# Performance work log

Measured on AMD Instinct MI355X. Metric: run time of the kernel, lower is better.

Reference implementation:

```python
import jax, jax.numpy as jnp
import numpy as np

COMMITMENT_COST = 0.25


def setup_inputs() -> dict:
    key = jax.random.key(0)
    k1, k2 = jax.random.split(key)
    inputs = jax.random.normal(k1, (16, 256, 32, 32), dtype=jnp.float32)
    embedding = jax.random.normal(k2, (8192, 256), dtype=jnp.float32)
    return {"inputs": inputs, "embedding": embedding}


def reference(inputs, embedding):
    # inputs: [B, C, H, W] with C == embedding_dim; embedding: [K, C]
    B, C, H, W = inputs.shape
    x = jnp.transpose(inputs, (0, 2, 3, 1))          # [B, H, W, C]
    flat = x.reshape(-1, C)                           # [N, C]
    # squared L2 distances: ||f||^2 + ||e||^2 - 2 f.e
    dist = (jnp.sum(flat * flat, axis=1, keepdims=True)
            + jnp.sum(embedding * embedding, axis=1)
            - 2.0 * flat @ embedding.T)               # [N, K]
    idx = jnp.argmin(dist, axis=1)                    # [N]
    quantized = embedding[idx].reshape(x.shape)       # [B, H, W, C]
    # commitment loss (eval mode: no EMA buffer updates)
    e_latent_loss = jnp.mean((jax.lax.stop_gradient(quantized) - x) ** 2)
    loss = COMMITMENT_COST * e_latent_loss
    # straight-through estimator
    q_st = x + jax.lax.stop_gradient(quantized - x)
    out = jnp.transpose(q_st, (0, 3, 1, 2))           # [B, C, H, W]
    return out, loss, idx.reshape(B, -1)
```

## Files before the change

### kernel.cpp

```cpp
#include <hip/hip_runtime.h>

#define C_   256
#define HW_  1024
#define N_   16384
#define K_   8192
#define OUT_SZ   4194304
#define LOSS_OFF 4194304
#define IDX_OFF  4194305
#define MARGIN   0.3f

typedef __attribute__((ext_vector_type(8)))  short short8;
typedef __attribute__((ext_vector_type(4)))  float f32x4;

#define REC_OFF    0u
#define CNORM_OFF  8388608u
#define NCNORM_OFF 8421376u
#define WS_NEED    8454144u

#define FB_CNORM   0u
#define FB_BESTS   32768u
#define FB_BESTK   557056u
#define FB_FIDX    1081344u

__device__ __forceinline__ unsigned short f2bf_rne(float x) {
  unsigned u = __float_as_uint(x);
  unsigned r = (u + 0x7fffu + ((u >> 16) & 1u)) >> 16;
  return (unsigned short)r;
}
__device__ __forceinline__ float bf2f(unsigned short h) {
  return __uint_as_float(((unsigned)h) << 16);
}
__device__ __forceinline__ void gld16(const void* g, void* l) {
  __builtin_amdgcn_global_load_lds((const __attribute__((address_space(1))) unsigned*)g,
                                   (__attribute__((address_space(3))) unsigned*)l, 16, 0, 0);
}
__device__ __forceinline__ float med3(float a, float b, float c) {
#if __has_builtin(__builtin_amdgcn_fmed3f)
  return __builtin_amdgcn_fmed3f(a, b, c);
#else
  return fmaxf(fminf(fmaxf(a, b), c), fminf(a, b));
#endif
}

__global__ __launch_bounds__(256) void conv_fused(const float* __restrict__ inp,
                                                  const float* __restrict__ emb,
                                                  unsigned short* __restrict__ Ah,
                                                  unsigned short* __restrict__ Bh,
                                                  float* __restrict__ cnorm,
                                                  float* __restrict__ ncnorm,
                                                  float* __restrict__ loss_slot) {
  __shared__ float T[64][65];
  int tid = threadIdx.x;
  if (blockIdx.x < 2048) {
    int wave = tid >> 6, lane = tid & 63;
    int k = blockIdx.x * 4 + wave;
    float4 v = *(const float4*)(emb + (size_t)k * C_ + lane * 4);
    float ss = v.x*v.x + v.y*v.y + v.z*v.z + v.w*v.w;
    #pragma unroll
    for (int m = 32; m > 0; m >>= 1) ss += __shfl_xor(ss, m);
    if (lane == 0) { cnorm[k] = 0.5f * ss; ncnorm[k] = -0.5f * ss; }
    uint2 p;
    p.x = (unsigned)f2bf_rne(v.x) | ((unsigned)f2bf_rne(v.y) << 16);
    p.y = (unsigned)f2bf_rne(v.z) | ((unsigned)f2bf_rne(v.w) << 16);
    *(uint2*)&Bh[(size_t)k * C_ + lane * 4] = p;
    if (blockIdx.x == 0 && tid == 0) { *loss_slot = 0.0f; }
  } else {
    int bb = blockIdx.x - 2048;
    int nt = bb >> 2, ct = bb & 3;
    int n0 = nt * 64, c0 = ct * 64;
    int b = n0 >> 10, hw0 = n0 & 1023;
    const float* base = inp + (size_t)b * (C_ * HW_) + hw0;
    #pragma unroll
    for (int i = 0; i < 4; ++i) {
      int cl = i * 16 + (tid >> 4);
      int h4 = (tid & 15) * 4;
      float4 v = *(const float4*)(base + (size_t)(c0 + cl) * HW_ + h4);
      T[h4 + 0][cl] = v.x; T[h4 + 1][cl] = v.y;
      T[h4 + 2][cl] = v.z; T[h4 + 3][cl] = v.w;
    }
    __syncthreads();
    #pragma unroll
    for (int jp = 0; jp < 2; ++jp) {
      int g = jp * 256 + tid;
      int nl = g >> 3, ch = (g & 7) * 8;
      unsigned short s8[8];
      #pragma unroll
      for (int k = 0; k < 8; ++k) s8[k] = f2bf_rne(T[nl][ch + k]);
      *(uint4*)&Ah[(size_t)(n0 + nl) * C_ + c0 + ch] = *(uint4*)s8;
    }
  }
}

__global__ __launch_bounds__(256, 2) void k_gemm1p(const unsigned short* __restrict__ Ah,
                                                   const unsigned short* __restrict__ Bh,
                                                   const float* __restrict__ ncnorm,
                                                   uint4* __restrict__ Rec) {
  __shared__ __align__(16) unsigned short LDS[3][12288];
  __shared__ __align__(16) float ncnL[1024];
  __shared__ float mS[2][128][3];

  const int tid = threadIdx.x, lane = tid & 63, wave = tid >> 6;
  const int wr = wave >> 1, wc = wave & 1;
  const int bid = (int)blockIdx.x;
  const int wg = (bid & 7) * 128 + (bid >> 3);
  const int rb = wg >> 3, kb = wg & 7;
  const int row0 = rb * 128;
  const int qm = lane & 15, quad = lane >> 4;
  const int sw = (quad ^ ((qm >> 1) & 3)) * 8;

  const char* srcA[2]; int dstA[2];
  #pragma unroll
  for (int t = 0; t < 2; ++t) {
    int g = t * 256 + tid;
    int row = g >> 2, chs = g & 3, ch = chs ^ ((row >> 1) & 3);
    srcA[t] = (const char*)Ah + (size_t)(row0 + row) * 512 + ch * 16;
    dstA[t] = g * 16;
  }
  const char* srcB[4]; int dstB[4];
  #pragma unroll
  for (int t = 0; t < 4; ++t) {
    int g = t * 256 + tid;
    int r = g >> 2, chs = g & 3, ch = chs ^ ((r >> 1) & 3);
    srcB[t] = (const char*)Bh + (size_t)(kb * 1024 + r) * 512 + ch * 16;
    dstB[t] = 8192 + g * 16;
  }

  gld16((const char*)ncnorm + (size_t)kb * 4096 + tid * 16, (char*)ncnL + tid * 16);
  #pragma unroll
  for (int t = 0; t < 2; ++t) gld16(srcA[t], (char*)LDS[0] + dstA[t]);
  #pragma unroll
  for (int t = 0; t < 4; ++t) gld16(srcB[t], (char*)LDS[0] + dstB[t]);
  #pragma unroll
  for (int t = 0; t < 2; ++t) gld16(srcA[t] + 64, (char*)LDS[1] + dstA[t]);
  #pragma unroll
  for (int t = 0; t < 4; ++t) gld16(srcB[t] + 64, (char*)LDS[1] + dstB[t]);
  asm volatile("s_waitcnt vmcnt(12)" ::: "memory");
  __builtin_amdgcn_s_barrier();

  const unsigned wq  = (unsigned)(wc * 128 + quad * 4);
  const unsigned kmk = 0xFFFFFF00u;

  int cur = 0, nst = 2;

  for (int sub = 0; sub < 4; ++sub) {
    const int nbe = kb * 4 + sub;
    const int nb4 = sub * 256 + wc * 128 + quad * 4;
    f32x4 acc[4][8];
    {
      float4 ncn[8];
      #pragma unroll
      for (int ct = 0; ct < 8; ++ct) ncn[ct] = *(const float4*)&ncnL[nb4 + ct * 16];
      #pragma unroll
      for (int r = 0; r < 4; ++r)
        #pragma unroll
        for (int c = 0; c < 8; ++c) {
          acc[r][c][0] = ncn[c].x; acc[r][c][1] = ncn[c].y;
          acc[r][c][2] = ncn[c].z; acc[r][c][3] = ncn[c].w;
        }
    }

    #pragma unroll 2
    for (int ci = 0; ci < 8; ++ci) {
      const int it = (sub << 3) | ci;
      if (it < 31) asm volatile("s_waitcnt vmcnt(6)" ::: "memory");
      else         asm volatile("s_waitcnt vmcnt(0)" ::: "memory");
      __builtin_amdgcn_s_barrier();
      __builtin_amdgcn_sched_barrier(0);

      if (it + 2 < 32) {
        const int nt2 = it + 2, nsub = nt2 >> 3, nci = nt2 & 7;
        #pragma unroll
        for (int t = 0; t < 2; ++t)
          gld16(srcA[t] + nci * 64, (char*)LDS[nst] + dstA[t]);
        #pragma unroll
        for (int t = 0; t < 4; ++t)
          gld16(srcB[t] + (size_t)nsub * 131072 + nci * 64, (char*)LDS[nst] + dstB[t]);
      }

      const unsigned short* Lb = &LDS[cur][0];
      short8 ah[4];
      #pragma unroll
      for (int rt = 0; rt < 4; ++rt) {
        int row = (wr * 4 + rt) * 16 + qm;
        ah[rt] = *(const short8*)&Lb[row * 32 + sw];
      }
      __builtin_amdgcn_s_setprio(1);
      #pragma unroll
      for (int ch2 = 0; ch2 < 2; ++ch2) {
        short8 bh[4];
        #pragma unroll
        for (int q = 0; q < 4; ++q) {
          int ct = ch2 * 4 + q;
          int r = (wc * 8 + ct) * 16 + qm;
          bh[q] = *(const short8*)&Lb[4096 + r * 32 + sw];
        }
        #pragma unroll
        for (int rt = 0; rt < 4; ++rt)
          #pragma unroll
          for (int q = 0; q < 4; ++q)
            acc[rt][ch2 * 4 + q] =
              __builtin_amdgcn_mfma_f32_16x16x32_bf16(bh[q], ah[rt], acc[rt][ch2 * 4 + q], 0, 0, 0);
      }
      __builtin_amdgcn_s_setprio(0);
      cur = (cur == 2) ? 0 : cur + 1;
      nst = (nst == 2) ? 0 : nst + 1;
    }

    #pragma unroll
    for (int rt = 0; rt < 4; ++rt) {
      float t1 = -3.4e38f, t2 = t1, t3 = t1;
      #pragma unroll
      for (int ct = 0; ct < 8; ++ct)
        #pragma unroll
        for (int rg = 0; rg < 4; ++rg) {
          unsigned idxv = wq | (unsigned)(ct * 16 + rg);
          float kf = __uint_as_float((__float_as_uint(acc[rt][ct][rg]) & kmk) | idxv);
          float n3 = med3(t2, kf, t3);
          float n2 = med3(t1, kf, t2);
          t1 = fmaxf(t1, kf);
          t2 = n2; t3 = n3;
        }
      #pragma unroll
      for (int m = 16; m < 64; m <<= 1) {
        float b1 = __shfl_xor(t1, m), b2 = __shfl_xor(t2, m), b3 = __shfl_xor(t3, m);
        float n3 = med3(t2, b1, t3);
        float n2 = med3(t1, b1, t2);
        t1 = fmaxf(t1, b1); t2 = n2; t3 = n3;
        n3 = med3(t2, b2, t3); t2 = fmaxf(t2, b2); t3 = n3;
        t3 = fmaxf(t3, b3);
      }
      if (quad == 0) {
        int rowl = wr * 64 + rt * 16 + qm;
        mS[wc][rowl][0] = t1; mS[wc][rowl][1] = t2; mS[wc][rowl][2] = t3;
      }
    }
    asm volatile("s_waitcnt lgkmcnt(0)" ::: "memory");
    __builtin_amdgcn_s_barrier();
    __builtin_amdgcn_sched_barrier(0);
    if (tid < 128) {
      float s1 = mS[0][tid][0], s2 = mS[0][tid][1], s3 = mS[0][tid][2];
      float b1 = mS[1][tid][0], b2 = mS[1][tid][1], b3 = mS[1][tid][2];
      float n3 = med3(s2, b1, s3);
      float n2 = med3(s1, b1, s2);
      s1 = fmaxf(s1, b1); s2 = n2; s3 = n3;
      n3 = med3(s2, b2, s3); s2 = fmaxf(s2, b2); s3 = n3;
      s3 = fmaxf(s3, b3);
      unsigned u1 = __float_as_uint(s1), u2 = __float_as_uint(s2), u3 = __float_as_uint(s3);
      uint4 rec;
      rec.x = u1 & kmk;
      rec.y = ((unsigned)f2bf_rne(__uint_as_float(u2 & kmk)) << 16)
            |  (unsigned)f2bf_rne(__uint_as_float(u3 & kmk));
      rec.z = (u1 & 255u) | ((u2 & 255u) << 8) | ((u3 & 255u) << 16);
      rec.w = 0u;
      Rec[(size_t)nbe * N_ + row0 + tid] = rec;
    }
  }
}

__global__ __launch_bounds__(256) void k_post(const float* __restrict__ inp,
                                              const float* __restrict__ emb,
                                              const float* __restrict__ cnorm,
                                              const uint4* __restrict__ Rec,
                                              float* __restrict__ out,
                                              float* __restrict__ outIdx,
                                              float* __restrict__ loss) {
  __shared__ float Q[16][258];
  __shared__ float gS[16];
  __shared__ int   ridx[16];
  __shared__ int   flist[16];
  __shared__ int   ckw[4][96];
  __shared__ float cscw[4][96];
  __shared__ int   ncw[4];
  __shared__ int   nflag;
  __shared__ float red[4];

  const int tid = threadIdx.x;
  const int n0 = blockIdx.x * 16, b = n0 >> 10, hw0 = n0 & 1023;
  const int lane = tid & 63, wv = tid >> 6;

  const int r = tid >> 4, j = tid & 15;
  const int row = n0 + r;
  uint4 rv[2];
  rv[0] = Rec[(size_t)(2 * j)     * N_ + row];
  rv[1] = Rec[(size_t)(2 * j + 1) * N_ + row];
  float m1 = -3.4e38f; int gk = 0x7fffffff;
  #pragma unroll
  for (int q = 0; q < 2; ++q) {
    float s1 = __uint_as_float(rv[q].x);
    int  kk = (2 * j + q) * 256 + (int)(rv[q].z & 255u);
    if (s1 > m1) { m1 = s1; gk = kk; }
  }
  #pragma unroll
  for (int m = 1; m < 16; m <<= 1) {
    float so = __shfl_xor(m1, m); int ko = __shfl_xor(gk, m);
    if (so > m1 || (so == m1 && ko < gk)) { m1 = so; gk = ko; }
  }
  float thr = m1 - MARGIN;
  int cnt = 0;
  #pragma unroll
  for (int q = 0; q < 2; ++q) {
    uint4 v = rv[q];
    cnt += (__uint_as_float(v.x) >= thr);
    cnt += (bf2f((unsigned short)(v.y >> 16)) >= thr);
    cnt += (bf2f((unsigned short)(v.y & 0xffffu)) >= thr);
  }
  #pragma unroll
  for (int m = 1; m < 16; m <<= 1) cnt += __shfl_xor(cnt, m);
  if (tid == 0) nflag = 0;
  __syncthreads();
  if (j == 0) {
    gS[r] = m1;
    if (cnt == 1) { ridx[r] = gk; }
    else { int p = atomicAdd(&nflag, 1); flist[p] = r; }
  }
  __syncthreads();

  int nf = nflag;
  for (int i = wv; i < nf; i += 4) {
    int lr = flist[i];
    int rw = n0 + lr;
    float fr[4];
    #pragma unroll
    for (int k = 0; k < 4; ++k)
      fr[k] = inp[(size_t)b * (C_ * HW_) + (size_t)(lane * 4 + k) * HW_ + (rw & 1023)];
    float th2 = gS[lr] - MARGIN;
    if (lane == 0) ncw[wv] = 0;
    if (lane < 32) {
      uint4 v = Rec[(size_t)lane * N_ + rw];
      float s1 = __uint_as_float(v.x);
      float s2 = bf2f((unsigned short)(v.y >> 16));
      float s3 = bf2f((unsigned short)(v.y & 0xffffu));
      int bb = lane * 256;
      if (s1 >= th2) { int p = atomicAdd(&ncw[wv], 1); ckw[wv][p] = bb + (int)(v.z & 255u); }
      if (s2 >= th2) { int p = atomicAdd(&ncw[wv], 1); ckw[wv][p] = bb + (int)((v.z >> 8) & 255u); }
      if (s3 >= th2) { int p = atomicAdd(&ncw[wv], 1); ckw[wv][p] = bb + (int)((v.z >> 16) & 255u); }
    }
    int nc = ncw[wv];
    for (int c = 0; c < nc; ++c) {
      int k = ckw[wv][c];
      float4 e = ((const float4*)(emb + (size_t)k * C_))[lane];
      float d = fr[0]*e.x + fr[1]*e.y + fr[2]*e.z + fr[3]*e.w;
      #pragma unroll
      for (int m = 32; m > 0; m >>= 1) d += __shfl_xor(d, m);
      if (lane == 0) cscw[wv][c] = d - cnorm[k];
    }
    if (lane == 0) {
      float bs = cscw[wv][0]; int bk = ckw[wv][0];
      for (int c = 1; c < nc; ++c)
        if (cscw[wv][c] > bs || (cscw[wv][c] == bs && ckw[wv][c] < bk)) { bs = cscw[wv][c]; bk = ckw[wv][c]; }
      ridx[lr] = bk;
    }
  }
  __syncthreads();

  if (tid < 16) outIdx[n0 + tid] = (float)ridx[tid];
  #pragma unroll
  for (int p = 0; p < 4; ++p) {
    int g = p * 256 + tid;
    int rr = g >> 6, c4 = (g & 63) * 4;
    int kq = ridx[rr];
    *(float4*)&Q[rr][c4] = *(const float4*)(emb + (size_t)kq * C_ + c4);
  }
  __syncthreads();

  float lsum = 0.0f;
  const int hw4 = (tid & 3) * 4, cl = tid >> 2;
  #pragma unroll
  for (int p = 0; p < 4; ++p) {
    int c = p * 64 + cl;
    size_t a = (size_t)b * (C_ * HW_) + (size_t)c * HW_ + hw0 + hw4;
    float4 x = *(const float4*)(inp + a);
    float4 q;
    q.x = Q[hw4 + 0][c]; q.y = Q[hw4 + 1][c];
    q.z = Q[hw4 + 2][c]; q.w = Q[hw4 + 3][c];
    *(float4*)(out + a) = q;
    float d0 = q.x - x.x, d1 = q.y - x.y, d2 = q.z - x.z, d3 = q.w - x.w;
    lsum += d0*d0 + d1*d1 + d2*d2 + d3*d3;
  }
  #pragma unroll
  for (int m = 32; m > 0; m >>= 1) lsum += __shfl_xor(lsum, m);
  if ((tid & 63) == 0) red[tid >> 6] = lsum;
  __syncthreads();
  if (tid == 0)
    atomicAdd(loss, (red[0] + red[1] + red[2] + red[3]) * (0.25f / (float)OUT_SZ));
}

__global__ __launch_bounds__(256) void k_norms_fb(const float* __restrict__ emb,
                                                  float* __restrict__ cnorm,
                                                  float* __restrict__ loss_slot) {
  int tid = threadIdx.x, wave = tid >> 6, lane = tid & 63;
  int k = blockIdx.x * 4 + wave;
  float4 v = *(const float4*)(emb + k * C_ + lane * 4);
  float s = v.x*v.x + v.y*v.y + v.z*v.z + v.w*v.w;
  #pragma unroll
  for (int m = 32; m > 0; m >>= 1) s += __shfl_xor(s, m);
  if (lane == 0) cnorm[k] = 0.5f * s;
  if (blockIdx.x == 0 && tid == 0) *loss_slot = 0.0f;
}

__global__ __launch_bounds__(256) void k_score_fb(const float* __restrict__ inp,
                                                  const float* __restrict__ emb,
                                                  const float* __restrict__ cnorm,
                                                  float* __restrict__ bestS,
                                                  int*   __restrict__ bestK) {
  __shared__ float As[16][132];
  __shared__ float Bs[16][132];
  const int tid = threadIdx.x;
  const int tx = tid & 15, ty = tid >> 4;
  const int rt = blockIdx.x >> 3, ks = blockIdx.x & 7;
  const int row0 = rt * 128;
  const float* Abase = inp + (row0 >> 10) * (C_ * HW_) + (row0 & 1023);
  const int kbase = ks * 1024;
  const int m4  = (tid & 31) << 2;
  const int ccA = tid >> 5;
  const int cc4 = (tid & 3) << 2;
  const int kkB = tid >> 2;

  float rS[8]; int rK[8];
  #pragma unroll
  for (int r = 0; r < 8; ++r) { rS[r] = -3.4e38f; rK[r] = 0; }

  for (int kt = 0; kt < 8; ++kt) {
    const int k0 = kbase + kt * 128;
    float acc[8][8];
    #pragma unroll
    for (int r = 0; r < 8; ++r)
      #pragma unroll
      for (int c = 0; c < 8; ++c) acc[r][c] = 0.f;

    for (int ci = 0; ci < 16; ++ci) {
      const int c0 = ci * 16;
      __syncthreads();
      #pragma unroll
      for (int p = 0; p < 2; ++p) {
        int cc = ccA + p * 8;
        float4 v = *(const float4*)(Abase + (c0 + cc) * HW_ + m4);
        *(float4*)(&As[cc][m4]) = v;
      }
      #pragma unroll
      for (int p = 0; p < 2; ++p) {
        int k = kkB + p * 64;
        float4 v = *(const float4*)(emb + (size_t)(k0 + k) * C_ + c0 + cc4);
        Bs[cc4 + 0][k] = v.x; Bs[cc4 + 1][k] = v.y;
        Bs[cc4 + 2][k] = v.z; Bs[cc4 + 3][k] = v.w;
      }
      __syncthreads();
      #pragma unroll
      for (int cc = 0; cc < 16; ++cc) {
        float4 a0 = *(const float4*)(&As[cc][ty * 8]);
        float4 a1 = *(const float4*)(&As[cc][ty * 8 + 4]);
        float4 b0 = *(const float4*)(&Bs[cc][tx * 8]);
        float4 b1 = *(const float4*)(&Bs[cc][tx * 8 + 4]);
        float a[8] = {a0.x, a0.y, a0.z, a0.w, a1.x, a1.y, a1.z, a1.w};
        float b[8] = {b0.x, b0.y, b0.z, b0.w, b1.x, b1.y, b1.z, b1.w};
        #pragma unroll
        for (int r = 0; r < 8; ++r)
          #pragma unroll
          for (int c = 0; c < 8; ++c) acc[r][c] += a[r] * b[c];
      }
    }
    float cn[8];
    {
      float4 c0v = *(const float4*)(cnorm + k0 + tx * 8);
      float4 c1v = *(const float4*)(cnorm + k0 + tx * 8 + 4);
      cn[0] = c0v.x; cn[1] = c0v.y; cn[2] = c0v.z; cn[3] = c0v.w;
      cn[4] = c1v.x; cn[5] = c1v.y; cn[6] = c1v.z; cn[7] = c1v.w;
    }
    #pragma unroll
    for (int r = 0; r < 8; ++r)
      #pragma unroll
      for (int c = 0; c < 8; ++c) {
        float s = acc[r][c] - cn[c];
        if (s > rS[r]) { rS[r] = s; rK[r] = k0 + tx * 8 + c; }
      }
  }
  #pragma unroll
  for (int r = 0; r < 8; ++r) {
    float s = rS[r]; int kk = rK[r];
    #pragma unroll
    for (int m = 1; m < 16; m <<= 1) {
      float so = __shfl_xor(s, m);
      int   ko = __shfl_xor(kk, m);
      if (so > s || (so == s && ko < kk)) { s = so; kk = ko; }
    }
    if (tx == 0) {
      int row = row0 + ty * 8 + r;
      bestS[ks * N_ + row] = s;
      bestK[ks * N_ + row] = kk;
    }
  }
}

__global__ __launch_bounds__(256) void k_merge_fb(const float* __restrict__ bestS,
                                                  const int*   __restrict__ bestK,
                                                  float* __restrict__ out_idx,
                                                  int*   __restrict__ fidx) {
  int n = blockIdx.x * 256 + threadIdx.x;
  float bs = -3.4e38f; int bk = 0x7fffffff;
  #pragma unroll
  for (int s = 0; s < 8; ++s) {
    float v = bestS[s * N_ + n];
    int  kk = bestK[s * N_ + n];
    if (v > bs || (v == bs && kk < bk)) { bs = v; bk = kk; }
  }
  out_idx[n] = (float)bk;
  fidx[n] = bk;
}

__global__ __launch_bounds__(256) void k_out_fb(const float* __restrict__ inp,
                                                const float* __restrict__ emb,
                                                const int* __restrict__ fidx,
                                                float* __restrict__ out,
                                                float* __restrict__ loss) {
  __shared__ float Q[32][260];
  int tid = threadIdx.x;
  int n0 = blockIdx.x * 32, b = n0 >> 10, hw0 = n0 & 1023;
  #pragma unroll
  for (int p = 0; p < 8; ++p) {
    int r = p * 4 + (tid >> 6);
    int kq = fidx[n0 + r];
    float4 v = *(const float4*)(emb + (size_t)kq * C_ + (tid & 63) * 4);
    *(float4*)&Q[r][(tid & 63) * 4] = v;
  }
  __syncthreads();
  int hwl = tid & 31, cl = tid >> 5;
  float lsum = 0.0f;
  #pragma unroll
  for (int p = 0; p < 32; ++p) {
    int c = p * 8 + cl;
    size_t a = (size_t)b * (C_ * HW_) + (size_t)c * HW_ + hw0 + hwl;
    float q = Q[hwl][c];
    float x = inp[a];
    out[a] = q;
    float dd = q - x; lsum += dd * dd;
  }
  #pragma unroll
  for (int m = 32; m > 0; m >>= 1) lsum += __shfl_xor(lsum, m);
  __shared__ float red[4];
  if ((tid & 63) == 0) red[tid >> 6] = lsum;
  __syncthreads();
  if (tid == 0)
    atomicAdd(loss, (red[0] + red[1] + red[2] + red[3]) * (0.25f / (float)OUT_SZ));
}

extern "C" void kernel_launch(void* const* d_in, const int* in_sizes, int n_in,
                              void* d_out, int out_size, void* d_ws, size_t ws_size,
                              hipStream_t stream) {
  const float* inp = (const float*)d_in[0];
  const float* emb = (const float*)d_in[1];
  float* out = (float*)d_out;
  char* ws = (char*)d_ws;

  if (ws_size >= (size_t)WS_NEED) {
    unsigned short* Ah = (unsigned short*)d_out;
    unsigned short* Bh = (unsigned short*)((char*)d_out + 8388608u);
    uint4* Rec     = (uint4*)(ws + REC_OFF);
    float* cnorm   = (float*)(ws + CNORM_OFF);
    float* ncnorm  = (float*)(ws + NCNORM_OFF);

    conv_fused <<<3072,  256, 0, stream>>>(inp, emb, Ah, Bh, cnorm, ncnorm,
                                           out + LOSS_OFF);
    k_gemm1p   <<<1024,  256, 0, stream>>>(Ah, Bh, ncnorm, Rec);
    k_post     <<<N_/16, 256, 0, stream>>>(inp, emb, cnorm, Rec, out,
                                           out + IDX_OFF, out + LOSS_OFF);
  } else {
    float* cnorm = (float*)(ws + FB_CNORM);
    float* bestS = (float*)(ws + FB_BESTS);
    int*   bestK = (int*)(ws + FB_BESTK);
    int*   fidx  = (int*)(ws + FB_FIDX);

    k_norms_fb <<<K_ / 4, 256, 0, stream>>>(emb, cnorm, out + LOSS_OFF);
    k_score_fb <<<1024,   256, 0, stream>>>(inp, emb, cnorm, bestS, bestK);
    k_merge_fb <<<N_/256, 256, 0, stream>>>(bestS, bestK, out + IDX_OFF, fidx);
    k_out_fb   <<<OUT_SZ/8192, 256, 0, stream>>>(inp, emb, fidx, out, out + LOSS_OFF);
  }
}
```

Baseline: 181.4 us.

## Compute commitment loss algebraically from input norms and best scores

The loss is now computed as sum ||x||^2 (accumulated in the transpose/convert kernel) minus twice the winning score, using ||q-x||^2 = ||x||^2 - 2(x.q - ||q||^2/2). This removes the re-read of the input in k_post. The k_post row-argmax reduction is also remapped so that rows lie across lanes and groups across waves, with an LDS merge step. The loss slot is now zeroed with a memset before the first kernel. In exchange, the loss for unambiguous rows uses the bf16/approximate GEMM score instead of an exact recompute, which risks precision error, and the change adds an extra memset launch.

```diff
diff --git a/kernel.cpp b/kernel.cpp
--- a/kernel.cpp
+++ b/kernel.cpp
@@ -48,8 +48,9 @@
                                                   unsigned short* __restrict__ Bh,
                                                   float* __restrict__ cnorm,
                                                   float* __restrict__ ncnorm,
-                                                  float* __restrict__ loss_slot) {
+                                                  float* __restrict__ loss) {
   __shared__ float T[64][65];
+  __shared__ float red[4];
   int tid = threadIdx.x;
   if (blockIdx.x < 2048) {
     int wave = tid >> 6, lane = tid & 63;
@@ -63,22 +64,28 @@
     p.x = (unsigned)f2bf_rne(v.x) | ((unsigned)f2bf_rne(v.y) << 16);
     p.y = (unsigned)f2bf_rne(v.z) | ((unsigned)f2bf_rne(v.w) << 16);
     *(uint2*)&Bh[(size_t)k * C_ + lane * 4] = p;
-    if (blockIdx.x == 0 && tid == 0) { *loss_slot = 0.0f; }
   } else {
     int bb = blockIdx.x - 2048;
     int nt = bb >> 2, ct = bb & 3;
     int n0 = nt * 64, c0 = ct * 64;
     int b = n0 >> 10, hw0 = n0 & 1023;
     const float* base = inp + (size_t)b * (C_ * HW_) + hw0;
+    float xsq = 0.0f;
     #pragma unroll
     for (int i = 0; i < 4; ++i) {
       int cl = i * 16 + (tid >> 4);
       int h4 = (tid & 15) * 4;
       float4 v = *(const float4*)(base + (size_t)(c0 + cl) * HW_ + h4);
+      xsq += v.x*v.x + v.y*v.y + v.z*v.z + v.w*v.w;
       T[h4 + 0][cl] = v.x; T[h4 + 1][cl] = v.y;
       T[h4 + 2][cl] = v.z; T[h4 + 3][cl] = v.w;
     }
+    #pragma unroll
+    for (int m = 32; m > 0; m >>= 1) xsq += __shfl_xor(xsq, m);
+    if ((tid & 63) == 0) red[tid >> 6] = xsq;
     __syncthreads();
+    if (tid == 0)
+      atomicAdd(loss, (red[0] + red[1] + red[2] + red[3]) * (0.25f / (float)OUT_SZ));
     #pragma unroll
     for (int jp = 0; jp < 2; ++jp) {
       int g = jp * 256 + tid;
@@ -265,53 +272,67 @@
                                               float* __restrict__ outIdx,
                                               float* __restrict__ loss) {
   __shared__ float Q[16][258];
+  __shared__ float wS[4][16];
+  __shared__ int   wK[4][16];
   __shared__ float gS[16];
+  __shared__ int   gK[16];
+  __shared__ int   sCnt[16];
+  __shared__ float sFin[16];
   __shared__ int   ridx[16];
   __shared__ int   flist[16];
   __shared__ int   ckw[4][96];
   __shared__ float cscw[4][96];
   __shared__ int   ncw[4];
   __shared__ int   nflag;
-  __shared__ float red[4];
 
   const int tid = threadIdx.x;
-  const int n0 = blockIdx.x * 16, b = n0 >> 10, hw0 = n0 & 1023;
+  const int n0 = blockIdx.x * 16, b = n0 >> 10;
   const int lane = tid & 63, wv = tid >> 6;
 
-  const int r = tid >> 4, j = tid & 15;
-  const int row = n0 + r;
-  uint4 rv[2];
-  rv[0] = Rec[(size_t)(2 * j)     * N_ + row];
-  rv[1] = Rec[(size_t)(2 * j + 1) * N_ + row];
-  float m1 = -3.4e38f; int gk = 0x7fffffff;
-  #pragma unroll
-  for (int q = 0; q < 2; ++q) {
-    float s1 = __uint_as_float(rv[q].x);
-    int  kk = (2 * j + q) * 256 + (int)(rv[q].z & 255u);
-    if (s1 > m1) { m1 = s1; gk = kk; }
-  }
-  #pragma unroll
-  for (int m = 1; m < 16; m <<= 1) {
+  const int r = tid & 15, g = tid >> 4;
+  uint4 rv0 = Rec[(size_t)(2 * g)     * N_ + n0 + r];
+  uint4 rv1 = Rec[(size_t)(2 * g + 1) * N_ + n0 + r];
+  float m1; int gk;
+  {
+    float s0 = __uint_as_float(rv0.x), s1 = __uint_as_float(rv1.x);
+    int  k0 = (2 * g) * 256 + (int)(rv0.z & 255u);
+    int  k1 = (2 * g + 1) * 256 + (int)(rv1.z & 255u);
+    m1 = s0; gk = k0;
+    if (s1 > m1) { m1 = s1; gk = k1; }
+  }
+  #pragma unroll
+  for (int m = 16; m < 64; m <<= 1) {
     float so = __shfl_xor(m1, m); int ko = __shfl_xor(gk, m);
     if (so > m1 || (so == m1 && ko < gk)) { m1 = so; gk = ko; }
   }
-  float thr = m1 - MARGIN;
-  int cnt = 0;
-  #pragma unroll
-  for (int q = 0; q < 2; ++q) {
-    uint4 v = rv[q];
-    cnt += (__uint_as_float(v.x) >= thr);
-    cnt += (bf2f((unsigned short)(v.y >> 16)) >= thr);
-    cnt += (bf2f((unsigned short)(v.y & 0xffffu)) >= thr);
-  }
-  #pragma unroll
-  for (int m = 1; m < 16; m <<= 1) cnt += __shfl_xor(cnt, m);
   if (tid == 0) nflag = 0;
-  __syncthreads();
-  if (j == 0) {
-    gS[r] = m1;
-    if (cnt == 1) { ridx[r] = gk; }
-    else { int p = atomicAdd(&nflag, 1); flist[p] = r; }
+  if (lane < 16) { wS[wv][r] = m1; wK[wv][r] = gk; }
+  __syncthreads();
+  if (tid < 16) {
+    float bm = wS[0][tid]; int bk = wK[0][tid];
+    #pragma unroll
+    for (int w = 1; w < 4; ++w) {
+      float so = wS[w][tid]; int ko = wK[w][tid];
+      if (so > bm || (so == bm && ko < bk)) { bm = so; bk = ko; }
+    }
+    gS[tid] = bm; gK[tid] = bk; sCnt[tid] = 0;
+  }
+  __syncthreads();
+  {
+    float thr = gS[r] - MARGIN;
+    int cnt = 0;
+    cnt += (__uint_as_float(rv0.x) >= thr);
+    cnt += (bf2f((unsigned short)(rv0.y >> 16)) >= thr);
+    cnt += (bf2f((unsigned short)(rv0.y & 0xffffu)) >= thr);
+    cnt += (__uint_as_float(rv1.x) >= thr);
+    cnt += (bf2f((unsigned short)(rv1.y >> 16)) >= thr);
+    cnt += (bf2f((unsigned short)(rv1.y & 0xffffu)) >= thr);
+    if (cnt) atomicAdd(&sCnt[r], cnt);
+  }
+  __syncthreads();
+  if (tid < 16) {
+    if (sCnt[tid] == 1) { ridx[tid] = gK[tid]; sFin[tid] = gS[tid]; }
+    else { int p = atomicAdd(&nflag, 1); flist[p] = tid; }
   }
   __syncthreads();
 
@@ -348,41 +369,38 @@
       float bs = cscw[wv][0]; int bk = ckw[wv][0];
       for (int c = 1; c < nc; ++c)
         if (cscw[wv][c] > bs || (cscw[wv][c] == bs && ckw[wv][c] < bk)) { bs = cscw[wv][c]; bk = ckw[wv][c]; }
-      ridx[lr] = bk;
-    }
-  }
-  __syncthreads();
-
-  if (tid < 16) outIdx[n0 + tid] = (float)ridx[tid];
+      ridx[lr] = bk; sFin[lr] = bs;
+    }
+  }
+  __syncthreads();
+
+  if (tid < 16) {
+    outIdx[n0 + tid] = (float)ridx[tid];
+    float sv = sFin[tid];
+    #pragma unroll
+    for (int m = 1; m < 16; m <<= 1) sv += __shfl_xor(sv, m);
+    if (tid == 0) atomicAdd(loss, sv * (-0.5f / (float)OUT_SZ));
+  }
   #pragma unroll
   for (int p = 0; p < 4; ++p) {
-    int g = p * 256 + tid;
-    int rr = g >> 6, c4 = (g & 63) * 4;
+    int gg = p * 256 + tid;
+    int rr = gg >> 6, c4 = (gg & 63) * 4;
     int kq = ridx[rr];
     *(float4*)&Q[rr][c4] = *(const float4*)(emb + (size_t)kq * C_ + c4);
   }
   __syncthreads();
 
-  float lsum = 0.0f;
   const int hw4 = (tid & 3) * 4, cl = tid >> 2;
+  const int hw0 = n0 & 1023;
   #pragma unroll
   for (int p = 0; p < 4; ++p) {
     int c = p * 64 + cl;
     size_t a = (size_t)b * (C_ * HW_) + (size_t)c * HW_ + hw0 + hw4;
-    float4 x = *(const float4*)(inp + a);
     float4 q;
     q.x = Q[hw4 + 0][c]; q.y = Q[hw4 + 1][c];
     q.z = Q[hw4 + 2][c]; q.w = Q[hw4 + 3][c];
     *(float4*)(out + a) = q;
-    float d0 = q.x - x.x, d1 = q.y - x.y, d2 = q.z - x.z, d3 = q.w - x.w;
-    lsum += d0*d0 + d1*d1 + d2*d2 + d3*d3;
-  }
-  #pragma unroll
-  for (int m = 32; m > 0; m >>= 1) lsum += __shfl_xor(lsum, m);
-  if ((tid & 63) == 0) red[tid >> 6] = lsum;
-  __syncthreads();
-  if (tid == 0)
-    atomicAdd(loss, (red[0] + red[1] + red[2] + red[3]) * (0.25f / (float)OUT_SZ));
+  }
 }
 
 __global__ __launch_bounds__(256) void k_norms_fb(const float* __restrict__ emb,
@@ -558,6 +576,8 @@
     float* cnorm   = (float*)(ws + CNORM_OFF);
     float* ncnorm  = (float*)(ws + NCNORM_OFF);
 
+    hipMemsetAsync((void*)(out + LOSS_OFF), 0, sizeof(float), stream);
+
     conv_fused <<<3072,  256, 0, stream>>>(inp, emb, Ah, Bh, cnorm, ncnorm,
                                            out + LOSS_OFF);
     k_gemm1p   <<<1024,  256, 0, stream>>>(Ah, Bh, ncnorm, Rec);
```

After: 190.8 us. +5.2%, slower.

## Enlarge distance GEMM tile to 256 rows with 8 waves and split-phase loads

Applied to the files above, without the earlier changes.

The distance GEMM workgroup grows from 256 to 512 threads, and its row tile grows from 128 to 256, so each loaded codebook tile is reused across twice as many input rows. The goal is to cut global and LDS traffic per MFMA. The inner loop is rewritten into two halves. Each half issues its share of the next-stage global-to-LDS copies (A, then B) between explicit barriers and LDS waits, interleaved with manually unrolled MFMA blocks. The cost is a larger LDS footprint, about 106 KB per block, which likely allows only one block per CU. It also adds two extra barriers per K step, which could expose latency.

```diff
diff --git a/kernel.cpp b/kernel.cpp
--- a/kernel.cpp
+++ b/kernel.cpp
@@ -91,50 +91,51 @@
   }
 }
 
-__global__ __launch_bounds__(256, 2) void k_gemm1p(const unsigned short* __restrict__ Ah,
+__global__ __launch_bounds__(512, 2) void k_gemm1p(const unsigned short* __restrict__ Ah,
                                                    const unsigned short* __restrict__ Bh,
                                                    const float* __restrict__ ncnorm,
                                                    uint4* __restrict__ Rec) {
-  __shared__ __align__(16) unsigned short LDS[3][12288];
+  __shared__ __align__(16) unsigned short LDS[3][16384];
   __shared__ __align__(16) float ncnL[1024];
-  __shared__ float mS[2][128][3];
+  __shared__ float mS[2][256][3];
 
   const int tid = threadIdx.x, lane = tid & 63, wave = tid >> 6;
   const int wr = wave >> 1, wc = wave & 1;
   const int bid = (int)blockIdx.x;
-  const int wg = (bid & 7) * 128 + (bid >> 3);
+  const int wg = (bid & 7) * 64 + (bid >> 3);
   const int rb = wg >> 3, kb = wg & 7;
-  const int row0 = rb * 128;
+  const int row0 = rb * 256;
   const int qm = lane & 15, quad = lane >> 4;
   const int sw = (quad ^ ((qm >> 1) & 3)) * 8;
 
   const char* srcA[2]; int dstA[2];
   #pragma unroll
   for (int t = 0; t < 2; ++t) {
-    int g = t * 256 + tid;
-    int row = g >> 2, chs = g & 3, ch = chs ^ ((row >> 1) & 3);
+    int c = t * 512 + tid;
+    int row = c >> 2, ch = (c & 3) ^ ((row >> 1) & 3);
     srcA[t] = (const char*)Ah + (size_t)(row0 + row) * 512 + ch * 16;
-    dstA[t] = g * 16;
-  }
-  const char* srcB[4]; int dstB[4];
-  #pragma unroll
-  for (int t = 0; t < 4; ++t) {
-    int g = t * 256 + tid;
-    int r = g >> 2, chs = g & 3, ch = chs ^ ((r >> 1) & 3);
+    dstA[t] = c * 16;
+  }
+  const char* srcB[2]; int dstB[2];
+  #pragma unroll
+  for (int t = 0; t < 2; ++t) {
+    int c = t * 512 + tid;
+    int r = c >> 2, ch = (c & 3) ^ ((r >> 1) & 3);
     srcB[t] = (const char*)Bh + (size_t)(kb * 1024 + r) * 512 + ch * 16;
-    dstB[t] = 8192 + g * 16;
-  }
-
-  gld16((const char*)ncnorm + (size_t)kb * 4096 + tid * 16, (char*)ncnL + tid * 16);
+    dstB[t] = 16384 + c * 16;
+  }
+
+  if (tid < 256)
+    gld16((const char*)ncnorm + (size_t)kb * 4096 + tid * 16, (char*)ncnL + tid * 16);
   #pragma unroll
   for (int t = 0; t < 2; ++t) gld16(srcA[t], (char*)LDS[0] + dstA[t]);
   #pragma unroll
-  for (int t = 0; t < 4; ++t) gld16(srcB[t], (char*)LDS[0] + dstB[t]);
+  for (int t = 0; t < 2; ++t) gld16(srcB[t], (char*)LDS[0] + dstB[t]);
   #pragma unroll
   for (int t = 0; t < 2; ++t) gld16(srcA[t] + 64, (char*)LDS[1] + dstA[t]);
   #pragma unroll
-  for (int t = 0; t < 4; ++t) gld16(srcB[t] + 64, (char*)LDS[1] + dstB[t]);
-  asm volatile("s_waitcnt vmcnt(12)" ::: "memory");
+  for (int t = 0; t < 2; ++t) gld16(srcB[t] + 64, (char*)LDS[1] + dstB[t]);
+  asm volatile("s_waitcnt vmcnt(8)" ::: "memory");
   __builtin_amdgcn_s_barrier();
 
   const unsigned wq  = (unsigned)(wc * 128 + quad * 4);
@@ -159,49 +160,84 @@
         }
     }
 
-    #pragma unroll 2
     for (int ci = 0; ci < 8; ++ci) {
       const int it = (sub << 3) | ci;
-      if (it < 31) asm volatile("s_waitcnt vmcnt(6)" ::: "memory");
+      if (it < 31) asm volatile("s_waitcnt vmcnt(4)" ::: "memory");
       else         asm volatile("s_waitcnt vmcnt(0)" ::: "memory");
       __builtin_amdgcn_s_barrier();
       __builtin_amdgcn_sched_barrier(0);
 
-      if (it + 2 < 32) {
-        const int nt2 = it + 2, nsub = nt2 >> 3, nci = nt2 & 7;
-        #pragma unroll
-        for (int t = 0; t < 2; ++t)
-          gld16(srcA[t] + nci * 64, (char*)LDS[nst] + dstA[t]);
-        #pragma unroll
-        for (int t = 0; t < 4; ++t)
-          gld16(srcB[t] + (size_t)nsub * 131072 + nci * 64, (char*)LDS[nst] + dstB[t]);
-      }
-
+      const bool st = (it + 2 < 32);
+      const int nt2 = it + 2, nsub = nt2 >> 3, nci = nt2 & 7;
+      char* stb = (char*)LDS[nst];
       const unsigned short* Lb = &LDS[cur][0];
-      short8 ah[4];
-      #pragma unroll
-      for (int rt = 0; rt < 4; ++rt) {
-        int row = (wr * 4 + rt) * 16 + qm;
-        ah[rt] = *(const short8*)&Lb[row * 32 + sw];
-      }
+      const size_t offB = (size_t)nsub * 131072 + (size_t)nci * 64;
+
+      short8 a0 = *(const short8*)&Lb[((wr * 4 + 0) * 16 + qm) * 32 + sw];
+      short8 a1 = *(const short8*)&Lb[((wr * 4 + 1) * 16 + qm) * 32 + sw];
+      short8 a2 = *(const short8*)&Lb[((wr * 4 + 2) * 16 + qm) * 32 + sw];
+      short8 a3 = *(const short8*)&Lb[((wr * 4 + 3) * 16 + qm) * 32 + sw];
+      short8 b0 = *(const short8*)&Lb[8192 + ((wc * 8 + 0) * 16 + qm) * 32 + sw];
+      short8 b1 = *(const short8*)&Lb[8192 + ((wc * 8 + 1) * 16 + qm) * 32 + sw];
+      short8 b2 = *(const short8*)&Lb[8192 + ((wc * 8 + 2) * 16 + qm) * 32 + sw];
+      short8 b3 = *(const short8*)&Lb[8192 + ((wc * 8 + 3) * 16 + qm) * 32 + sw];
+      if (st) {
+        gld16(srcA[0] + nci * 64, stb + dstA[0]);
+        gld16(srcA[1] + nci * 64, stb + dstA[1]);
+      }
+      __builtin_amdgcn_s_barrier();
+      asm volatile("s_waitcnt lgkmcnt(0)" ::: "memory");
+      __builtin_amdgcn_sched_barrier(0);
       __builtin_amdgcn_s_setprio(1);
-      #pragma unroll
-      for (int ch2 = 0; ch2 < 2; ++ch2) {
-        short8 bh[4];
-        #pragma unroll
-        for (int q = 0; q < 4; ++q) {
-          int ct = ch2 * 4 + q;
-          int r = (wc * 8 + ct) * 16 + qm;
-          bh[q] = *(const short8*)&Lb[4096 + r * 32 + sw];
-        }
-        #pragma unroll
-        for (int rt = 0; rt < 4; ++rt)
-          #pragma unroll
-          for (int q = 0; q < 4; ++q)
-            acc[rt][ch2 * 4 + q] =
-              __builtin_amdgcn_mfma_f32_16x16x32_bf16(bh[q], ah[rt], acc[rt][ch2 * 4 + q], 0, 0, 0);
-      }
+      acc[0][0] = __builtin_amdgcn_mfma_f32_16x16x32_bf16(b0, a0, acc[0][0], 0, 0, 0);
+      acc[0][1] = __builtin_amdgcn_mfma_f32_16x16x32_bf16(b1, a0, acc[0][1], 0, 0, 0);
+      acc[0][2] = __builtin_amdgcn_mfma_f32_16x16x32_bf16(b2, a0, acc[0][2], 0, 0, 0);
+      acc[0][3] = __builtin_amdgcn_mfma_f32_16x16x32_bf16(b3, a0, acc[0][3], 0, 0, 0);
+      acc[1][0] = __builtin_amdgcn_mfma_f32_16x16x32_bf16(b0, a1, acc[1][0], 0, 0, 0);
+      acc[1][1] = __builtin_amdgcn_mfma_f32_16x16x32_bf16(b1, a1, acc[1][1], 0, 0, 0);
+      acc[1][2] = __builtin_amdgcn_mfma_f32_16x16x32_bf16(b2, a1, acc[1][2], 0, 0, 0);
+      acc[1][3] = __builtin_amdgcn_mfma_f32_16x16x32_bf16(b3, a1, acc[1][3], 0, 0, 0);
+      acc[2][0] = __builtin_amdgcn_mfma_f32_16x16x32_bf16(b0, a2, acc[2][0], 0, 0, 0);
+      acc[2][1] = __builtin_amdgcn_mfma_f32_16x16x32_bf16(b1, a2, acc[2][1], 0, 0, 0);
+      acc[2][2] = __builtin_amdgcn_mfma_f32_16x16x32_bf16(b2, a2, acc[2][2], 0, 0, 0);
+      acc[2][3] = __builtin_amdgcn_mfma_f32_16x16x32_bf16(b3, a2, acc[2][3], 0, 0, 0);
+      acc[3][0] = __builtin_amdgcn_mfma_f32_16x16x32_bf16(b0, a3, acc[3][0], 0, 0, 0);
+      acc[3][1] = __builtin_amdgcn_mfma_f32_16x16x32_bf16(b1, a3, acc[3][1], 0, 0, 0);
+      acc[3][2] = __builtin_amdgcn_mfma_f32_16x16x32_bf16(b2, a3, acc[3][2], 0, 0, 0);
+      acc[3][3] = __builtin_amdgcn_mfma_f32_16x16x32_bf16(b3, a3, acc[3][3], 0, 0, 0);
       __builtin_amdgcn_s_setprio(0);
+      __builtin_amdgcn_s_barrier();
+
+      short8 b4 = *(const short8*)&Lb[8192 + ((wc * 8 + 4) * 16 + qm) * 32 + sw];
+      short8 b5 = *(const short8*)&Lb[8192 + ((wc * 8 + 5) * 16 + qm) * 32 + sw];
+      short8 b6 = *(const short8*)&Lb[8192 + ((wc * 8 + 6) * 16 + qm) * 32 + sw];
+      short8 b7 = *(const short8*)&Lb[8192 + ((wc * 8 + 7) * 16 + qm) * 32 + sw];
+      if (st) {
+        gld16(srcB[0] + offB, stb + dstB[0]);
+        gld16(srcB[1] + offB, stb + dstB[1]);
+      }
+      __builtin_amdgcn_s_barrier();
+      asm volatile("s_waitcnt lgkmcnt(0)" ::: "memory");
+      __builtin_amdgcn_sched_barrier(0);
+      __builtin_amdgcn_s_setprio(1);
+      acc[0][4] = __builtin_amdgcn_mfma_f32_16x16x32_bf16(b4, a0, acc[0][4], 0, 0, 0);
+      acc[0][5] = __builtin_amdgcn_mfma_f32_16x16x32_bf16(b5, a0, acc[0][5], 0, 0, 0);
+      acc[0][6] = __builtin_amdgcn_mfma_f32_16x16x32_bf16(b6, a0, acc[0][6], 0, 0, 0);
+      acc[0][7] = __builtin_amdgcn_mfma_f32_16x16x32_bf16(b7, a0, acc[0][7], 0, 0, 0);
+      acc[1][4] = __builtin_amdgcn_mfma_f32_16x16x32_bf16(b4, a1, acc[1][4], 0, 0, 0);
+      acc[1][5] = __builtin_amdgcn_mfma_f32_16x16x32_bf16(b5, a1, acc[1][5], 0, 0, 0);
+      acc[1][6] = __builtin_amdgcn_mfma_f32_16x16x32_bf16(b6, a1, acc[1][6], 0, 0, 0);
+      acc[1][7] = __builtin_amdgcn_mfma_f32_16x16x32_bf16(b7, a1, acc[1][7], 0, 0, 0);
+      acc[2][4] = __builtin_amdgcn_mfma_f32_16x16x32_bf16(b4, a2, acc[2][4], 0, 0, 0);
+      acc[2][5] = __builtin_amdgcn_mfma_f32_16x16x32_bf16(b5, a2, acc[2][5], 0, 0, 0);
+      acc[2][6] = __builtin_amdgcn_mfma_f32_16x16x32_bf16(b6, a2, acc[2][6], 0, 0, 0);
+      acc[2][7] = __builtin_amdgcn_mfma_f32_16x16x32_bf16(b7, a2, acc[2][7], 0, 0, 0);
+      acc[3][4] = __builtin_amdgcn_mfma_f32_16x16x32_bf16(b4, a3, acc[3][4], 0, 0, 0);
+      acc[3][5] = __builtin_amdgcn_mfma_f32_16x16x32_bf16(b5, a3, acc[3][5], 0, 0, 0);
+      acc[3][6] = __builtin_amdgcn_mfma_f32_16x16x32_bf16(b6, a3, acc[3][6], 0, 0, 0);
+      acc[3][7] = __builtin_amdgcn_mfma_f32_16x16x32_bf16(b7, a3, acc[3][7], 0, 0, 0);
+      __builtin_amdgcn_s_setprio(0);
+
       cur = (cur == 2) ? 0 : cur + 1;
       nst = (nst == 2) ? 0 : nst + 1;
     }
@@ -237,7 +273,7 @@
     asm volatile("s_waitcnt lgkmcnt(0)" ::: "memory");
     __builtin_amdgcn_s_barrier();
     __builtin_amdgcn_sched_barrier(0);
-    if (tid < 128) {
+    if (tid < 256) {
       float s1 = mS[0][tid][0], s2 = mS[0][tid][1], s3 = mS[0][tid][2];
       float b1 = mS[1][tid][0], b2 = mS[1][tid][1], b3 = mS[1][tid][2];
       float n3 = med3(s2, b1, s3);
@@ -560,7 +596,7 @@
 
     conv_fused <<<3072,  256, 0, stream>>>(inp, emb, Ah, Bh, cnorm, ncnorm,
                                            out + LOSS_OFF);
-    k_gemm1p   <<<1024,  256, 0, stream>>>(Ah, Bh, ncnorm, Rec);
+    k_gemm1p   <<<512,   512, 0, stream>>>(Ah, Bh, ncnorm, Rec);
     k_post     <<<N_/16, 256, 0, stream>>>(inp, emb, cnorm, Rec, out,
                                            out + IDX_OFF, out + LOSS_OFF);
   } else {
```

New measurement: 232.7 us. +28.2%, slower.
